# Kernel tuning notes

Hardware: AMD Instinct MI355X
Metric: run time of the kernel (lower is better)

## Reference

```python
import jax, jax.numpy as jnp
import numpy as np

VOCAB = 32000
HID = 1024
HEADS = 16
HEAD_DIM = HID // HEADS
LAYERS = 8
INTER = 4 * HID
ROPE_BASE = 100000.0
EPS = 1e-5


def setup_inputs() -> dict:
    key = jax.random.key(0)
    ks = jax.random.split(key, 12)
    s = 0.02
    inp = {
        'input_ids': jax.random.randint(ks[0], (2, 2048), 0, VOCAB),
        'embed_W': jax.random.normal(ks[1], (VOCAB, HID), jnp.float32) * s,
        'Wq': jax.random.normal(ks[2], (LAYERS, HID, HID), jnp.float32) * s,
        'Wk': jax.random.normal(ks[3], (LAYERS, HID, HID), jnp.float32) * s,
        'Wv': jax.random.normal(ks[4], (LAYERS, HID, HID), jnp.float32) * s,
        'Wo': jax.random.normal(ks[5], (LAYERS, HID, HID), jnp.float32) * s,
        'Wg': jax.random.normal(ks[6], (LAYERS, HID, INTER), jnp.float32) * s,
        'Wu': jax.random.normal(ks[7], (LAYERS, HID, INTER), jnp.float32) * s,
        'Wd': jax.random.normal(ks[8], (LAYERS, INTER, HID), jnp.float32) * s,
        'norm1_w': jnp.ones((LAYERS, HID), jnp.float32),
        'norm2_w': jnp.ones((LAYERS, HID), jnp.float32),
        'final_norm_w': jnp.ones((HID,), jnp.float32),
        'head_W': jax.random.normal(ks[9], (HID, VOCAB), jnp.float32) * s,
    }
    return inp


def rms_norm(x, w):
    return x * jax.lax.rsqrt(jnp.mean(x * x, axis=-1, keepdims=True) + EPS) * w


def rope_tables(seq_len):
    freq = 1.0 / (ROPE_BASE ** (jnp.arange(0, HEAD_DIM, 2, dtype=jnp.float32) / HEAD_DIM))
    ang = jnp.arange(seq_len, dtype=jnp.float32)[:, None] * freq  # [S, d/2]
    cos = jnp.concatenate([jnp.cos(ang), jnp.cos(ang)], axis=-1)  # [S, d]
    sin = jnp.concatenate([jnp.sin(ang), jnp.sin(ang)], axis=-1)
    return cos, sin


def rotate_half(x):
    h = x.shape[-1] // 2
    return jnp.concatenate([-x[..., h:], x[..., :h]], axis=-1)


def apply_rope(q, k, cos, sin):
    # q,k: [B,S,H,D]; cos,sin: [S,D] -> broadcast over heads via [:,None,:]
    c = cos[:, None, :]
    s = sin[:, None, :]
    return q * c + rotate_half(q) * s, k * c + rotate_half(k) * s


def attention(x, wq, wk, wv, wo, cos, sin, causal_mask):
    B, S, _ = x.shape
    q = (x @ wq).reshape(B, S, HEADS, HEAD_DIM)
    k = (x @ wk).reshape(B, S, HEADS, HEAD_DIM)
    v = (x @ wv).reshape(B, S, HEADS, HEAD_DIM)
    q, k = apply_rope(q, k, cos, sin)
    scores = jnp.einsum('bqhd,bkhd->bhqk', q, k) / np.sqrt(HEAD_DIM)
    scores = jnp.clip(scores, -1000.0, 1000.0)
    scores = jnp.where(causal_mask, jnp.finfo(scores.dtype).min, scores)
    w = jax.nn.softmax(scores.astype(jnp.float32), axis=-1).astype(q.dtype)
    w = jnp.clip(w, 0.0, 1.0)
    ctx = jnp.einsum('bhqk,bkhd->bqhd', w, v).reshape(B, S, HID)
    return ctx @ wo


def reference(input_ids, embed_W, Wq, Wk, Wv, Wo, Wg, Wu, Wd, norm1_w, norm2_w, final_norm_w, head_W):
    B, S = input_ids.shape
    h = embed_W[input_ids]  # [B,S,HID]
    cos, sin = rope_tables(S)
    causal_mask = jnp.triu(jnp.ones((S, S), bool), k=1)[None, None]
    for l in range(LAYERS):
        h = h + attention(rms_norm(h, norm1_w[l]), Wq[l], Wk[l], Wv[l], Wo[l], cos, sin, causal_mask)
        hn = rms_norm(h, norm2_w[l])
        h = h + (jax.nn.silu(hn @ Wg[l]) * (hn @ Wu[l])) @ Wd[l]
    h = rms_norm(h, final_norm_w)
    logits = h @ head_W
    return logits, h
```

## Files before the change

kernel.cpp:

```cpp
#include <hip/hip_runtime.h>

#define T_TOK 4096
#define SEQ   2048
#define HID   1024
#define NH    16
#define HD    64
#define INTER 4096
#define NLAYER 8
#define VOCAB 32000

typedef short short8 __attribute__((ext_vector_type(8)));
typedef float f32x4  __attribute__((ext_vector_type(4)));

__device__ __forceinline__ unsigned short f2bf(float f){
  unsigned int u = __builtin_bit_cast(unsigned int, f);
  u += 0x7fffu + ((u >> 16) & 1u);
  return (unsigned short)(u >> 16);
}
__device__ __forceinline__ float bf2f(unsigned short b){
  unsigned int u = ((unsigned int)b) << 16;
  return __builtin_bit_cast(float, u);
}

#define GLOAD_LDS16(gsrc, ldst) \
  __builtin_amdgcn_global_load_lds((const __attribute__((address_space(1))) void*)(gsrc), \
                                   (__attribute__((address_space(3))) void*)(ldst), 16, 0, 0)

__global__ __launch_bounds__(256) void embed_kernel(const int* __restrict__ ids,
                                                    const float* __restrict__ W,
                                                    float* __restrict__ h){
  int i = blockIdx.x * 256 + threadIdx.x;
  int t = i >> 8, c = i & 255;
  ((float4*)h)[i] = ((const float4*)(W + (size_t)ids[t] * HID))[c];
}

__global__ __launch_bounds__(256) void rope_tab_kernel(float* __restrict__ cosT,
                                                       float* __restrict__ sinT){
  int i = blockIdx.x * 256 + threadIdx.x;
  int s = i >> 5, f = i & 31;
  float inv = expf(-((2.0f * (float)f) / 64.0f) * logf(100000.0f));
  float ang = (float)s * inv;
  cosT[i] = cosf(ang);
  sinT[i] = sinf(ang);
}

__global__ __launch_bounds__(256) void rmsnorm_kernel(const float* __restrict__ h,
                                                      const float* __restrict__ w,
                                                      unsigned short* __restrict__ out,
                                                      float* hcopy){
  int t = blockIdx.x, tid = threadIdx.x;
  float4 v = ((const float4*)(h + (size_t)t * HID))[tid];
  float ss = v.x*v.x + v.y*v.y + v.z*v.z + v.w*v.w;
  #pragma unroll
  for (int m = 1; m < 64; m <<= 1) ss += __shfl_xor(ss, m);
  __shared__ float red[4];
  if ((tid & 63) == 0) red[tid >> 6] = ss;
  __syncthreads();
  float r = rsqrtf((red[0] + red[1] + red[2] + red[3]) * (1.0f / HID) + 1e-5f);
  float4 wv = ((const float4*)w)[tid];
  float nx = v.x * r * wv.x;
  float ny = v.y * r * wv.y;
  float nz = v.z * r * wv.z;
  float nw = v.w * r * wv.w;
  ushort4 o;
  o.x = f2bf(nx); o.y = f2bf(ny); o.z = f2bf(nz); o.w = f2bf(nw);
  ((ushort4*)(out + (size_t)t * HID))[tid] = o;
  if (hcopy){
    float4 hv; hv.x = nx; hv.y = ny; hv.z = nz; hv.w = nw;
    ((float4*)(hcopy + (size_t)t * HID))[tid] = hv;
  }
}

__global__ __launch_bounds__(256) void rope_kernel(unsigned short* __restrict__ q,
                                                   unsigned short* __restrict__ k,
                                                   const float* __restrict__ cosT,
                                                   const float* __restrict__ sinT){
  int i = blockIdx.x * 256 + threadIdx.x;
  int t = i >> 9, rem = i & 511;
  int hh = rem >> 5, f = rem & 31;
  int s = t & (SEQ - 1);
  float c = cosT[s * 32 + f], sn = sinT[s * 32 + f];
  size_t base = (size_t)t * HID + hh * HD + f;
  float q0 = bf2f(q[base]), q1 = bf2f(q[base + 32]);
  q[base]      = f2bf((q0 * c - q1 * sn) * 0.125f);
  q[base + 32] = f2bf((q1 * c + q0 * sn) * 0.125f);
  float k0 = bf2f(k[base]), k1 = bf2f(k[base + 32]);
  k[base]      = f2bf(k0 * c - k1 * sn);
  k[base + 32] = f2bf(k1 * c + k0 * sn);
}

__global__ __launch_bounds__(256) void convert_w_kernel(const float* __restrict__ W,
                                                        unsigned short* __restrict__ Wt,
                                                        int K, int N){
  __shared__ unsigned short t_lds[64][72];
  W  += (size_t)blockIdx.z * K * N;
  Wt += (size_t)blockIdx.z * K * N;
  const int n0 = blockIdx.x * 64, k0 = blockIdx.y * 64;
  const int tid = threadIdx.x;
  const int tr = tid >> 4, tc = tid & 15;
  #pragma unroll
  for (int i = 0; i < 4; ++i){
    int kk = tr + i * 16;
    float4 v = *(const float4*)(W + (size_t)(k0 + kk) * N + n0 + tc * 4);
    t_lds[tc*4+0][kk] = f2bf(v.x);
    t_lds[tc*4+1][kk] = f2bf(v.y);
    t_lds[tc*4+2][kk] = f2bf(v.z);
    t_lds[tc*4+3][kk] = f2bf(v.w);
  }
  __syncthreads();
  const int n = tid >> 2, cp = tid & 3;
  #pragma unroll
  for (int j = 0; j < 2; ++j){
    int c = cp * 2 + j;
    uint4 d = *(const uint4*)(&t_lds[n][c * 8]);
    *(uint4*)(Wt + (size_t)(n0 + n) * K + k0 + c * 8) = d;
  }
}

__device__ __forceinline__ void gemm_core(const unsigned short* __restrict__ A,
                                          const unsigned short* __restrict__ Bt,
                                          int Kstride, int Klen, int m0, int n0,
                                          unsigned short* As, unsigned short* Bs,
                                          f32x4 (&acc)[4][4]){
  const int tid = threadIdx.x;
  const int lane = tid & 63, w = tid >> 6;
  const int l15 = lane & 15, g = lane >> 4;
  const int wr = w >> 1, wc = w & 1;
  const int srow = lane >> 2;
  const int schunk = (((lane & 3) ^ ((srow >> 1) & 3)) << 3);
  const int sx = (l15 >> 1) & 3;

  #pragma unroll
  for (int m = 0; m < 4; ++m)
    #pragma unroll
    for (int n = 0; n < 4; ++n)
      #pragma unroll
      for (int i = 0; i < 4; ++i) acc[m][n][i] = 0.0f;

  for (int kk = 0; kk < Klen; kk += 32){
    __syncthreads();
    GLOAD_LDS16(A  + (size_t)(m0 +      w*16 + srow) * Kstride + kk + schunk, As + (w*16) * 32);
    GLOAD_LDS16(A  + (size_t)(m0 + 64 + w*16 + srow) * Kstride + kk + schunk, As + (64 + w*16) * 32);
    GLOAD_LDS16(Bt + (size_t)(n0 +      w*16 + srow) * Kstride + kk + schunk, Bs + (w*16) * 32);
    GLOAD_LDS16(Bt + (size_t)(n0 + 64 + w*16 + srow) * Kstride + kk + schunk, Bs + (64 + w*16) * 32);
    __syncthreads();
    short8 a[4], b[4];
    #pragma unroll
    for (int m = 0; m < 4; ++m)
      a[m] = *(const short8*)(As + (wr*64 + m*16 + l15) * 32 + ((g ^ sx) << 3));
    #pragma unroll
    for (int n = 0; n < 4; ++n)
      b[n] = *(const short8*)(Bs + (wc*64 + n*16 + l15) * 32 + ((g ^ sx) << 3));
    #pragma unroll
    for (int m = 0; m < 4; ++m)
      #pragma unroll
      for (int n = 0; n < 4; ++n)
        acc[m][n] = __builtin_amdgcn_mfma_f32_16x16x32_bf16(a[m], b[n], acc[m][n], 0, 0, 0);
  }
}

template<int MODE>
__device__ __forceinline__ void gemm_epi(const f32x4 (&acc)[4][4], void* Cout,
                                         const float* __restrict__ resid,
                                         int N, int m0, int n0, int ldt){
  const int tid = threadIdx.x;
  const int lane = tid & 63, w = tid >> 6;
  const int l15 = lane & 15, g = lane >> 4;
  const int wr = w >> 1, wc = w & 1;
  #pragma unroll
  for (int m = 0; m < 4; ++m){
    #pragma unroll
    for (int n = 0; n < 4; ++n){
      int row0 = m0 + wr * 64 + m * 16 + g * 4;
      int col  = n0 + wc * 64 + n * 16 + l15;
      #pragma unroll
      for (int i = 0; i < 4; ++i){
        float v = acc[m][n][i];
        if (MODE == 0){
          ((unsigned short*)Cout)[(size_t)(row0 + i) * N + col] = f2bf(v);
        } else if (MODE == 1){
          size_t idx = (size_t)(row0 + i) * N + col;
          ((float*)Cout)[idx] = resid[idx] + v;
        } else if (MODE == 2){
          ((unsigned short*)Cout)[(size_t)col * ldt + (row0 + i)] = f2bf(v);
        } else if (MODE == 3){
          __builtin_nontemporal_store(v, &((float*)Cout)[(size_t)(row0 + i) * N + col]);
        } else {
          atomicAdd(&((float*)Cout)[(size_t)(row0 + i) * N + col], v);
        }
      }
    }
  }
}

template<int MODE>
__global__ __launch_bounds__(256) void gemm_bf16(const unsigned short* __restrict__ A,
                                                 const unsigned short* __restrict__ Bt,
                                                 void* Cout, const float* resid,
                                                 int K, int N, int ldt){
  __shared__ unsigned short As[128 * 32];
  __shared__ unsigned short Bs[128 * 32];
  f32x4 acc[4][4];
  gemm_core(A, Bt, K, K, blockIdx.x * 128, blockIdx.y * 128, As, Bs, acc);
  gemm_epi<MODE>(acc, Cout, resid, N, blockIdx.x * 128, blockIdx.y * 128, ldt);
}

__global__ __launch_bounds__(256) void gemm_splitk(const unsigned short* __restrict__ A,
                                                   const unsigned short* __restrict__ Bt,
                                                   float* Cacc, int Kfull, int N){
  __shared__ unsigned short As[128 * 32];
  __shared__ unsigned short Bs[128 * 32];
  const int kh = blockIdx.z, khalf = Kfull >> 1;
  f32x4 acc[4][4];
  gemm_core(A + kh * khalf, Bt + kh * khalf, Kfull, khalf,
            blockIdx.x * 128, blockIdx.y * 128, As, Bs, acc);
  gemm_epi<4>(acc, Cacc, nullptr, N, blockIdx.x * 128, blockIdx.y * 128, 0);
}

__global__ __launch_bounds__(256) void gemm_qkv(const unsigned short* __restrict__ A,
                                                const unsigned short* __restrict__ BtQ,
                                                const unsigned short* __restrict__ BtK,
                                                const unsigned short* __restrict__ BtV,
                                                unsigned short* qb, unsigned short* kb,
                                                unsigned short* vt){
  __shared__ unsigned short As[128 * 32];
  __shared__ unsigned short Bs[128 * 32];
  const int nb = blockIdx.y, sel = nb >> 3, n0 = (nb & 7) * 128;
  const unsigned short* Bt = (sel == 0) ? BtQ : (sel == 1) ? BtK : BtV;
  f32x4 acc[4][4];
  gemm_core(A, Bt, HID, HID, blockIdx.x * 128, n0, As, Bs, acc);
  if (sel == 0)      gemm_epi<0>(acc, qb, nullptr, HID, blockIdx.x * 128, n0, 0);
  else if (sel == 1) gemm_epi<0>(acc, kb, nullptr, HID, blockIdx.x * 128, n0, 0);
  else               gemm_epi<2>(acc, vt, nullptr, HID, blockIdx.x * 128, n0, T_TOK);
}

__global__ __launch_bounds__(256) void gemm_gu(const unsigned short* __restrict__ A,
                                               const unsigned short* __restrict__ BtG,
                                               const unsigned short* __restrict__ BtU,
                                               unsigned short* gb, unsigned short* ub){
  __shared__ unsigned short As[128 * 32];
  __shared__ unsigned short Bs[128 * 32];
  const int nb = blockIdx.y, sel = nb >> 5, n0 = (nb & 31) * 128;
  f32x4 acc[4][4];
  gemm_core(A, sel ? BtU : BtG, HID, HID, blockIdx.x * 128, n0, As, Bs, acc);
  gemm_epi<0>(acc, sel ? ub : gb, nullptr, INTER, blockIdx.x * 128, n0, 0);
}

__global__ __launch_bounds__(256, 2) void gemm_f32b(const unsigned short* __restrict__ A,
                                                    const float* __restrict__ Bw,
                                                    float* __restrict__ Cout,
                                                    int M, int N, int K){
  __shared__ unsigned short As[128 * 32];
  __shared__ unsigned short Bs[128 * 32];
  const int tid = threadIdx.x;
  const int lane = tid & 63, wid = tid >> 6;
  const int l15 = lane & 15, g = lane >> 4;
  const int wr = wid >> 1, wc = wid & 1;
  const int m0 = blockIdx.x * 128, n0 = blockIdx.y * 128;
  const int bcol = tid & 127, bhalf = tid >> 7;
  f32x4 acc[4][4];
  #pragma unroll
  for (int m = 0; m < 4; ++m)
    #pragma unroll
    for (int n = 0; n < 4; ++n)
      #pragma unroll
      for (int i = 0; i < 4; ++i) acc[m][n][i] = 0.0f;
  for (int kk = 0; kk < K; kk += 32){
    __syncthreads();
    #pragma unroll
    for (int cc = 0; cc < 2; ++cc){
      int c = tid + cc * 256;
      int row = c >> 2, kc = (c & 3) << 3;
      uint4 d = *(const uint4*)(A + (size_t)(m0 + row) * K + kk + kc);
      *(uint4*)(&As[row * 32 + kc]) = d;
    }
    {
      const float* bp = Bw + (size_t)(kk + bhalf * 16) * N + n0 + bcol;
      float f[16];
      #pragma unroll
      for (int j = 0; j < 16; ++j) f[j] = bp[(size_t)j * N];
      unsigned int pk[8];
      #pragma unroll
      for (int j = 0; j < 8; ++j)
        pk[j] = (unsigned int)f2bf(f[2*j]) | ((unsigned int)f2bf(f[2*j+1]) << 16);
      int sw = (bcol >> 1) & 3;
      int c0 = ((bhalf << 1)     ) ^ sw;
      int c1 = ((bhalf << 1) | 1 ) ^ sw;
      uint4 w0; w0.x = pk[0]; w0.y = pk[1]; w0.z = pk[2]; w0.w = pk[3];
      uint4 w1; w1.x = pk[4]; w1.y = pk[5]; w1.z = pk[6]; w1.w = pk[7];
      *(uint4*)(&Bs[bcol * 32 + c0 * 8]) = w0;
      *(uint4*)(&Bs[bcol * 32 + c1 * 8]) = w1;
    }
    __syncthreads();
    short8 a[4], b[4];
    #pragma unroll
    for (int m = 0; m < 4; ++m)
      a[m] = *(const short8*)(&As[(wr*64 + m*16 + l15) * 32 + g*8]);
    #pragma unroll
    for (int n = 0; n < 4; ++n){
      int col = wc*64 + n*16 + l15;
      b[n] = *(const short8*)(&Bs[col * 32 + (g ^ ((col >> 1) & 3)) * 8]);
    }
    #pragma unroll
    for (int m = 0; m < 4; ++m)
      #pragma unroll
      for (int n = 0; n < 4; ++n)
        acc[m][n] = __builtin_amdgcn_mfma_f32_16x16x32_bf16(a[m], b[n], acc[m][n], 0, 0, 0);
  }
  #pragma unroll
  for (int m = 0; m < 4; ++m)
    #pragma unroll
    for (int n = 0; n < 4; ++n){
      int row0 = m0 + wr*64 + m*16 + g*4;
      int col  = n0 + wc*64 + n*16 + l15;
      #pragma unroll
      for (int i = 0; i < 4; ++i)
        Cout[(size_t)(row0 + i) * N + col] = acc[m][n][i];
    }
}

__global__ __launch_bounds__(256) void attn_kernel(const unsigned short* __restrict__ q,
                                                   const unsigned short* __restrict__ k,
                                                   const unsigned short* __restrict__ vt,
                                                   unsigned short* __restrict__ ctx){
  const int tid = threadIdx.x;
  const int lane = tid & 63, w = tid >> 6;
  const int l15 = lane & 15, g = lane >> 4;
  const int bx = (int)gridDim.x - 1 - (int)blockIdx.x;
  const int q0 = bx * 128 + w * 32;
  const int hh = blockIdx.y;
  const int tb = blockIdx.z * SEQ;

  __shared__ unsigned short Ks[64][72];
  __shared__ unsigned short Vs[64][72];
  __shared__ unsigned short Ps[4][16][72];

  short8 qa[2][2];
  #pragma unroll
  for (int qs = 0; qs < 2; ++qs)
    #pragma unroll
    for (int kd = 0; kd < 2; ++kd)
      qa[qs][kd] = *(const short8*)(q + (size_t)(tb + q0 + qs*16 + l15) * HID + hh*HD + kd*32 + g*8);

  float m_run[2][4], l_run[2][4];
  f32x4 o_acc[2][4];
  #pragma unroll
  for (int qs = 0; qs < 2; ++qs)
    #pragma unroll
    for (int i = 0; i < 4; ++i){ m_run[qs][i] = -1e30f; l_run[qs][i] = 0.0f; }
  #pragma unroll
  for (int qs = 0; qs < 2; ++qs)
    #pragma unroll
    for (int dt = 0; dt < 4; ++dt)
      #pragma unroll
      for (int i = 0; i < 4; ++i) o_acc[qs][dt][i] = 0.0f;

  const int ntile = 2 * bx + 2;
  const int srow = tid >> 2, sc = (tid & 3) * 16;
  const unsigned short* kbase = k  + (size_t)(tb + srow) * HID + hh*HD + sc;
  const unsigned short* vbase = vt + (size_t)(hh*HD + srow) * T_TOK + tb + sc;

  for (int kt = 0; kt < ntile; ++kt){
    const int kv0 = kt * 64;
    __syncthreads();
    {
      const unsigned short* kp = kbase + (size_t)kv0 * HID;
      const unsigned short* vp = vbase + kv0;
      *(uint4*)(&Ks[srow][sc])     = *(const uint4*)(kp);
      *(uint4*)(&Ks[srow][sc + 8]) = *(const uint4*)(kp + 8);
      *(uint4*)(&Vs[srow][sc])     = *(const uint4*)(vp);
      *(uint4*)(&Vs[srow][sc + 8]) = *(const uint4*)(vp + 8);
    }
    __syncthreads();
    const int nct = min(4, ((q0 + 31 - kv0) >> 4) + 1);
    if (nct <= 0) continue;
    const int nks = nct >> 1;

    #pragma unroll
    for (int qs = 0; qs < 2; ++qs){
      float pv[4][4];
      #pragma unroll
      for (int ct = 0; ct < 4; ++ct){
        if (ct < nct){
          f32x4 scv;
          #pragma unroll
          for (int i = 0; i < 4; ++i) scv[i] = 0.0f;
          scv = __builtin_amdgcn_mfma_f32_16x16x32_bf16(qa[qs][0],
                  *(const short8*)(&Ks[ct*16 + l15][g*8]), scv, 0, 0, 0);
          scv = __builtin_amdgcn_mfma_f32_16x16x32_bf16(qa[qs][1],
                  *(const short8*)(&Ks[ct*16 + l15][32 + g*8]), scv, 0, 0, 0);
          #pragma unroll
          for (int i = 0; i < 4; ++i){
            float s = fminf(fmaxf(scv[i], -1000.0f), 1000.0f);
            int row = q0 + qs*16 + g*4 + i;
            int col = kv0 + ct*16 + l15;
            pv[ct][i] = (col > row) ? -1e30f : s;
          }
        } else {
          #pragma unroll
          for (int i = 0; i < 4; ++i) pv[ct][i] = -1e30f;
        }
      }
      #pragma unroll
      for (int i = 0; i < 4; ++i){
        float mx = fmaxf(fmaxf(pv[0][i], pv[1][i]), fmaxf(pv[2][i], pv[3][i]));
        #pragma unroll
        for (int msk = 1; msk < 16; msk <<= 1) mx = fmaxf(mx, __shfl_xor(mx, msk));
        if (!__all(mx <= m_run[qs][i] + 8.0f)){
          float mnew = fmaxf(m_run[qs][i], mx);
          float scale = __expf(m_run[qs][i] - mnew);
          m_run[qs][i] = mnew;
          l_run[qs][i] *= scale;
          #pragma unroll
          for (int dt = 0; dt < 4; ++dt) o_acc[qs][dt][i] *= scale;
        }
        float psum = 0.0f;
        #pragma unroll
        for (int ct = 0; ct < 4; ++ct){
          if (ct < nct){
            float p = __expf(pv[ct][i] - m_run[qs][i]);
            pv[ct][i] = p; psum += p;
          } else pv[ct][i] = 0.0f;
        }
        #pragma unroll
        for (int msk = 1; msk < 16; msk <<= 1) psum += __shfl_xor(psum, msk);
        l_run[qs][i] += psum;
      }
      #pragma unroll
      for (int ct = 0; ct < 4; ++ct)
        if (ct < nct)
          #pragma unroll
          for (int i = 0; i < 4; ++i)
            Ps[w][g*4 + i][ct*16 + l15] = f2bf(pv[ct][i]);
      #pragma unroll
      for (int ks = 0; ks < 2; ++ks){
        if (ks < nks){
          short8 ap = *(const short8*)(&Ps[w][l15][ks*32 + g*8]);
          #pragma unroll
          for (int dt = 0; dt < 4; ++dt){
            short8 vb = *(const short8*)(&Vs[dt*16 + l15][ks*32 + g*8]);
            o_acc[qs][dt] = __builtin_amdgcn_mfma_f32_16x16x32_bf16(ap, vb, o_acc[qs][dt], 0, 0, 0);
          }
        }
      }
    }
  }
  #pragma unroll
  for (int qs = 0; qs < 2; ++qs)
    #pragma unroll
    for (int dt = 0; dt < 4; ++dt)
      #pragma unroll
      for (int i = 0; i < 4; ++i){
        float o = o_acc[qs][dt][i] / l_run[qs][i];
        ctx[(size_t)(tb + q0 + qs*16 + g*4 + i) * HID + hh*HD + dt*16 + l15] = f2bf(o);
      }
}

__global__ __launch_bounds__(256) void silu_mul_kernel(unsigned short* __restrict__ gbuf,
                                                       const unsigned short* __restrict__ ubuf){
  int i = blockIdx.x * 256 + threadIdx.x;
  ushort4 gv = ((const ushort4*)gbuf)[i];
  ushort4 uv = ((const ushort4*)ubuf)[i];
  ushort4 o;
  float x;
  x = bf2f(gv.x); o.x = f2bf((x / (1.0f + __expf(-x))) * bf2f(uv.x));
  x = bf2f(gv.y); o.y = f2bf((x / (1.0f + __expf(-x))) * bf2f(uv.y));
  x = bf2f(gv.z); o.z = f2bf((x / (1.0f + __expf(-x))) * bf2f(uv.z));
  x = bf2f(gv.w); o.w = f2bf((x / (1.0f + __expf(-x))) * bf2f(uv.w));
  ((ushort4*)gbuf)[i] = o;
}

extern "C" void kernel_launch(void* const* d_in, const int* in_sizes, int n_in,
                              void* d_out, int out_size, void* d_ws, size_t ws_size,
                              hipStream_t stream){
  const int*   ids    = (const int*)d_in[0];
  const float* embedW = (const float*)d_in[1];
  const float* Wq = (const float*)d_in[2];
  const float* Wk = (const float*)d_in[3];
  const float* Wv = (const float*)d_in[4];
  const float* Wo = (const float*)d_in[5];
  const float* Wg = (const float*)d_in[6];
  const float* Wu = (const float*)d_in[7];
  const float* Wd = (const float*)d_in[8];
  const float* n1 = (const float*)d_in[9];
  const float* n2 = (const float*)d_in[10];
  const float* nf = (const float*)d_in[11];
  const float* Wh = (const float*)d_in[12];
  float* out = (float*)d_out;

  char* scb = (char*)d_out;
  unsigned short* qb  = (unsigned short*)(scb + 0);
  unsigned short* kb  = (unsigned short*)(scb + 8388608);
  unsigned short* vtb = (unsigned short*)(scb + 16777216);
  unsigned short* ctx = (unsigned short*)(scb + 25165824);
  unsigned short* gb  = (unsigned short*)(scb + 33554432);
  unsigned short* ub  = (unsigned short*)(scb + 67108864);
  float* cosT = (float*)(scb + 100663296);
  float* sinT = (float*)(scb + 100925440);
  float* h_fallback   = (float*)(scb + 104857600);
  unsigned short* WtQ = (unsigned short*)(scb + 134217728);
  unsigned short* WtK = (unsigned short*)(scb + 150994944);
  unsigned short* WtV = (unsigned short*)(scb + 167772160);
  unsigned short* WtO = (unsigned short*)(scb + 184549376);
  unsigned short* WtG = (unsigned short*)(scb + 201326592);
  unsigned short* WtU = (unsigned short*)(scb + 268435456);
  unsigned short* WtD = (unsigned short*)(scb + 335544320);

  unsigned short* xn = (unsigned short*)d_ws;
  float* h = (ws_size >= 25165824u) ? (float*)((char*)d_ws + 8388608) : h_fallback;
  unsigned short* WhT = (ws_size >= 90701824u)
                      ? (unsigned short*)((char*)d_ws + 25165824) : nullptr;

  convert_w_kernel<<<dim3(16, 16, 8), 256, 0, stream>>>(Wq, WtQ, HID, HID);
  convert_w_kernel<<<dim3(16, 16, 8), 256, 0, stream>>>(Wk, WtK, HID, HID);
  convert_w_kernel<<<dim3(16, 16, 8), 256, 0, stream>>>(Wv, WtV, HID, HID);
  convert_w_kernel<<<dim3(16, 16, 8), 256, 0, stream>>>(Wo, WtO, HID, HID);
  convert_w_kernel<<<dim3(64, 16, 8), 256, 0, stream>>>(Wg, WtG, HID, INTER);
  convert_w_kernel<<<dim3(64, 16, 8), 256, 0, stream>>>(Wu, WtU, HID, INTER);
  convert_w_kernel<<<dim3(16, 64, 8), 256, 0, stream>>>(Wd, WtD, INTER, HID);
  if (WhT)
    convert_w_kernel<<<dim3(500, 16, 1), 256, 0, stream>>>(Wh, WhT, HID, VOCAB);

  embed_kernel<<<4096, 256, 0, stream>>>(ids, embedW, h);
  rope_tab_kernel<<<256, 256, 0, stream>>>(cosT, sinT);

  for (int l = 0; l < NLAYER; ++l){
    rmsnorm_kernel<<<4096, 256, 0, stream>>>(h, n1 + l*HID, xn, nullptr);
    gemm_qkv<<<dim3(32, 24), 256, 0, stream>>>(xn, WtQ + (size_t)l*HID*HID,
                                               WtK + (size_t)l*HID*HID,
                                               WtV + (size_t)l*HID*HID, qb, kb, vtb);
    rope_kernel<<<8192, 256, 0, stream>>>(qb, kb, cosT, sinT);
    attn_kernel<<<dim3(16, 16, 2), 256, 0, stream>>>(qb, kb, vtb, ctx);
    gemm_splitk<<<dim3(32, 8, 2), 256, 0, stream>>>(ctx, WtO + (size_t)l*HID*HID,
                                                    h, HID, HID);
    rmsnorm_kernel<<<4096, 256, 0, stream>>>(h, n2 + l*HID, xn, nullptr);
    gemm_gu<<<dim3(32, 64), 256, 0, stream>>>(xn, WtG + (size_t)l*HID*INTER,
                                              WtU + (size_t)l*HID*INTER, gb, ub);
    silu_mul_kernel<<<16384, 256, 0, stream>>>(gb, ub);
    gemm_splitk<<<dim3(32, 8, 2), 256, 0, stream>>>(gb, WtD + (size_t)l*HID*INTER,
                                                    h, INTER, HID);
  }

  rmsnorm_kernel<<<4096, 256, 0, stream>>>(h, nf, xn, out + 131072000);
  if (WhT)
    gemm_bf16<3><<<dim3(32, 250), 256, 0, stream>>>(xn, WhT, out, nullptr, HID, VOCAB, 0);
  else
    gemm_f32b<<<dim3(32, 250), 256, 0, stream>>>(xn, Wh, out, T_TOK, VOCAB, HID);
}
```

Before: 4.089 ms.

## Use K=64 GEMM tiles with pre-swizzled weights, drop split-K atomics

Adds a GEMM core that stages 64-wide K slices per iteration, which halves the number of barrier pairs. The weights are stored pre-swizzled at conversion time so the B tile can be loaded linearly into LDS without bank conflicts, while A is swizzled at load. The O-projection and down-projection switch from split-K with atomicAdd to a single pass with a fused residual add. The LM head grid is reordered so blocks sweep the vocab dimension first. In exchange, LDS use doubles and the two residual GEMMs launch only 256 blocks each, which lowers parallelism.

```diff
diff --git a/kernel.cpp b/kernel.cpp
--- a/kernel.cpp
+++ b/kernel.cpp
@@ -89,9 +89,9 @@
   k[base + 32] = f2bf(k1 * c + k0 * sn);
 }
 
-__global__ __launch_bounds__(256) void convert_w_kernel(const float* __restrict__ W,
-                                                        unsigned short* __restrict__ Wt,
-                                                        int K, int N){
+__global__ __launch_bounds__(256) void convert_w_swz(const float* __restrict__ W,
+                                                     unsigned short* __restrict__ Wt,
+                                                     int K, int N){
   __shared__ unsigned short t_lds[64][72];
   W  += (size_t)blockIdx.z * K * N;
   Wt += (size_t)blockIdx.z * K * N;
@@ -113,15 +113,94 @@
   for (int j = 0; j < 2; ++j){
     int c = cp * 2 + j;
     uint4 d = *(const uint4*)(&t_lds[n][c * 8]);
+    *(uint4*)(Wt + (size_t)(n0 + n) * K + k0 + ((c ^ (n & 7)) << 3)) = d;
+  }
+}
+
+__global__ __launch_bounds__(256) void convert_w_lin(const float* __restrict__ W,
+                                                     unsigned short* __restrict__ Wt,
+                                                     int K, int N){
+  __shared__ unsigned short t_lds[64][72];
+  const int n0 = blockIdx.x * 64, k0 = blockIdx.y * 64;
+  const int tid = threadIdx.x;
+  const int tr = tid >> 4, tc = tid & 15;
+  #pragma unroll
+  for (int i = 0; i < 4; ++i){
+    int kk = tr + i * 16;
+    float4 v = *(const float4*)(W + (size_t)(k0 + kk) * N + n0 + tc * 4);
+    t_lds[tc*4+0][kk] = f2bf(v.x);
+    t_lds[tc*4+1][kk] = f2bf(v.y);
+    t_lds[tc*4+2][kk] = f2bf(v.z);
+    t_lds[tc*4+3][kk] = f2bf(v.w);
+  }
+  __syncthreads();
+  const int n = tid >> 2, cp = tid & 3;
+  #pragma unroll
+  for (int j = 0; j < 2; ++j){
+    int c = cp * 2 + j;
+    uint4 d = *(const uint4*)(&t_lds[n][c * 8]);
     *(uint4*)(Wt + (size_t)(n0 + n) * K + k0 + c * 8) = d;
   }
 }
 
-__device__ __forceinline__ void gemm_core(const unsigned short* __restrict__ A,
-                                          const unsigned short* __restrict__ Bt,
-                                          int Kstride, int Klen, int m0, int n0,
-                                          unsigned short* As, unsigned short* Bs,
-                                          f32x4 (&acc)[4][4]){
+__device__ __forceinline__ void gemm_core64(const unsigned short* __restrict__ A,
+                                            const unsigned short* __restrict__ Bt,
+                                            int K, int m0, int n0,
+                                            unsigned short* As, unsigned short* Bs,
+                                            f32x4 (&acc)[4][4]){
+  const int tid = threadIdx.x;
+  const int lane = tid & 63, w = tid >> 6;
+  const int l15 = lane & 15, g = lane >> 4;
+  const int lr = lane >> 3;
+  const int lc = lane & 7;
+  const int wr = w >> 1, wc = w & 1;
+  const int axor = ((lc ^ lr) << 3);
+
+  #pragma unroll
+  for (int m = 0; m < 4; ++m)
+    #pragma unroll
+    for (int n = 0; n < 4; ++n)
+      #pragma unroll
+      for (int i = 0; i < 4; ++i) acc[m][n][i] = 0.0f;
+
+  for (int kk = 0; kk < K; kk += 64){
+    __syncthreads();
+    #pragma unroll
+    for (int i = 0; i < 4; ++i){
+      int rb = (i * 4 + w) * 8;
+      GLOAD_LDS16(A  + (size_t)(m0 + rb + lr) * K + kk + axor,      As + rb * 64);
+      GLOAD_LDS16(Bt + (size_t)(n0 + rb + lr) * K + kk + (lc << 3), Bs + rb * 64);
+    }
+    __syncthreads();
+    short8 a[4][2], b[4][2];
+    const int x = l15 & 7;
+    #pragma unroll
+    for (int m = 0; m < 4; ++m){
+      int row = wr * 64 + m * 16 + l15;
+      a[m][0] = *(const short8*)(As + row * 64 + ((g       ^ x) << 3));
+      a[m][1] = *(const short8*)(As + row * 64 + (((4 + g) ^ x) << 3));
+    }
+    #pragma unroll
+    for (int n = 0; n < 4; ++n){
+      int row = wc * 64 + n * 16 + l15;
+      b[n][0] = *(const short8*)(Bs + row * 64 + ((g       ^ x) << 3));
+      b[n][1] = *(const short8*)(Bs + row * 64 + (((4 + g) ^ x) << 3));
+    }
+    #pragma unroll
+    for (int m = 0; m < 4; ++m)
+      #pragma unroll
+      for (int n = 0; n < 4; ++n){
+        acc[m][n] = __builtin_amdgcn_mfma_f32_16x16x32_bf16(a[m][0], b[n][0], acc[m][n], 0, 0, 0);
+        acc[m][n] = __builtin_amdgcn_mfma_f32_16x16x32_bf16(a[m][1], b[n][1], acc[m][n], 0, 0, 0);
+      }
+  }
+}
+
+__device__ __forceinline__ void gemm_core32(const unsigned short* __restrict__ A,
+                                            const unsigned short* __restrict__ Bt,
+                                            int K, int m0, int n0,
+                                            unsigned short* As, unsigned short* Bs,
+                                            f32x4 (&acc)[4][4]){
   const int tid = threadIdx.x;
   const int lane = tid & 63, w = tid >> 6;
   const int l15 = lane & 15, g = lane >> 4;
@@ -137,12 +216,12 @@
       #pragma unroll
       for (int i = 0; i < 4; ++i) acc[m][n][i] = 0.0f;
 
-  for (int kk = 0; kk < Klen; kk += 32){
-    __syncthreads();
-    GLOAD_LDS16(A  + (size_t)(m0 +      w*16 + srow) * Kstride + kk + schunk, As + (w*16) * 32);
-    GLOAD_LDS16(A  + (size_t)(m0 + 64 + w*16 + srow) * Kstride + kk + schunk, As + (64 + w*16) * 32);
-    GLOAD_LDS16(Bt + (size_t)(n0 +      w*16 + srow) * Kstride + kk + schunk, Bs + (w*16) * 32);
-    GLOAD_LDS16(Bt + (size_t)(n0 + 64 + w*16 + srow) * Kstride + kk + schunk, Bs + (64 + w*16) * 32);
+  for (int kk = 0; kk < K; kk += 32){
+    __syncthreads();
+    GLOAD_LDS16(A  + (size_t)(m0 +      w*16 + srow) * K + kk + schunk, As + (w*16) * 32);
+    GLOAD_LDS16(A  + (size_t)(m0 + 64 + w*16 + srow) * K + kk + schunk, As + (64 + w*16) * 32);
+    GLOAD_LDS16(Bt + (size_t)(n0 +      w*16 + srow) * K + kk + schunk, Bs + (w*16) * 32);
+    GLOAD_LDS16(Bt + (size_t)(n0 + 64 + w*16 + srow) * K + kk + schunk, Bs + (64 + w*16) * 32);
     __syncthreads();
     short8 a[4], b[4];
     #pragma unroll
@@ -183,10 +262,8 @@
           ((float*)Cout)[idx] = resid[idx] + v;
         } else if (MODE == 2){
           ((unsigned short*)Cout)[(size_t)col * ldt + (row0 + i)] = f2bf(v);
-        } else if (MODE == 3){
+        } else {
           __builtin_nontemporal_store(v, &((float*)Cout)[(size_t)(row0 + i) * N + col]);
-        } else {
-          atomicAdd(&((float*)Cout)[(size_t)(row0 + i) * N + col], v);
         }
       }
     }
@@ -194,27 +271,15 @@
 }
 
 template<int MODE>
-__global__ __launch_bounds__(256) void gemm_bf16(const unsigned short* __restrict__ A,
-                                                 const unsigned short* __restrict__ Bt,
-                                                 void* Cout, const float* resid,
-                                                 int K, int N, int ldt){
-  __shared__ unsigned short As[128 * 32];
-  __shared__ unsigned short Bs[128 * 32];
+__global__ __launch_bounds__(256) void gemm64_k(const unsigned short* __restrict__ A,
+                                                const unsigned short* __restrict__ Bt,
+                                                void* Cout, const float* resid,
+                                                int K, int N, int ldt){
+  __shared__ unsigned short As[128 * 64];
+  __shared__ unsigned short Bs[128 * 64];
   f32x4 acc[4][4];
-  gemm_core(A, Bt, K, K, blockIdx.x * 128, blockIdx.y * 128, As, Bs, acc);
+  gemm_core64(A, Bt, K, blockIdx.x * 128, blockIdx.y * 128, As, Bs, acc);
   gemm_epi<MODE>(acc, Cout, resid, N, blockIdx.x * 128, blockIdx.y * 128, ldt);
-}
-
-__global__ __launch_bounds__(256) void gemm_splitk(const unsigned short* __restrict__ A,
-                                                   const unsigned short* __restrict__ Bt,
-                                                   float* Cacc, int Kfull, int N){
-  __shared__ unsigned short As[128 * 32];
-  __shared__ unsigned short Bs[128 * 32];
-  const int kh = blockIdx.z, khalf = Kfull >> 1;
-  f32x4 acc[4][4];
-  gemm_core(A + kh * khalf, Bt + kh * khalf, Kfull, khalf,
-            blockIdx.x * 128, blockIdx.y * 128, As, Bs, acc);
-  gemm_epi<4>(acc, Cacc, nullptr, N, blockIdx.x * 128, blockIdx.y * 128, 0);
 }
 
 __global__ __launch_bounds__(256) void gemm_qkv(const unsigned short* __restrict__ A,
@@ -223,12 +288,12 @@
                                                 const unsigned short* __restrict__ BtV,
                                                 unsigned short* qb, unsigned short* kb,
                                                 unsigned short* vt){
-  __shared__ unsigned short As[128 * 32];
-  __shared__ unsigned short Bs[128 * 32];
+  __shared__ unsigned short As[128 * 64];
+  __shared__ unsigned short Bs[128 * 64];
   const int nb = blockIdx.y, sel = nb >> 3, n0 = (nb & 7) * 128;
   const unsigned short* Bt = (sel == 0) ? BtQ : (sel == 1) ? BtK : BtV;
   f32x4 acc[4][4];
-  gemm_core(A, Bt, HID, HID, blockIdx.x * 128, n0, As, Bs, acc);
+  gemm_core64(A, Bt, HID, blockIdx.x * 128, n0, As, Bs, acc);
   if (sel == 0)      gemm_epi<0>(acc, qb, nullptr, HID, blockIdx.x * 128, n0, 0);
   else if (sel == 1) gemm_epi<0>(acc, kb, nullptr, HID, blockIdx.x * 128, n0, 0);
   else               gemm_epi<2>(acc, vt, nullptr, HID, blockIdx.x * 128, n0, T_TOK);
@@ -238,12 +303,23 @@
                                                const unsigned short* __restrict__ BtG,
                                                const unsigned short* __restrict__ BtU,
                                                unsigned short* gb, unsigned short* ub){
+  __shared__ unsigned short As[128 * 64];
+  __shared__ unsigned short Bs[128 * 64];
+  const int nb = blockIdx.y, sel = nb >> 5, n0 = (nb & 31) * 128;
+  f32x4 acc[4][4];
+  gemm_core64(A, sel ? BtU : BtG, HID, blockIdx.x * 128, n0, As, Bs, acc);
+  gemm_epi<0>(acc, sel ? ub : gb, nullptr, INTER, blockIdx.x * 128, n0, 0);
+}
+
+__global__ __launch_bounds__(256) void gemm_head(const unsigned short* __restrict__ A,
+                                                 const unsigned short* __restrict__ Bt,
+                                                 float* __restrict__ out){
   __shared__ unsigned short As[128 * 32];
   __shared__ unsigned short Bs[128 * 32];
-  const int nb = blockIdx.y, sel = nb >> 5, n0 = (nb & 31) * 128;
+  const int m0 = blockIdx.y * 128, n0 = blockIdx.x * 128;
   f32x4 acc[4][4];
-  gemm_core(A, sel ? BtU : BtG, HID, HID, blockIdx.x * 128, n0, As, Bs, acc);
-  gemm_epi<0>(acc, sel ? ub : gb, nullptr, INTER, blockIdx.x * 128, n0, 0);
+  gemm_core32(A, Bt, HID, m0, n0, As, Bs, acc);
+  gemm_epi<3>(acc, out, nullptr, VOCAB, m0, n0, 0);
 }
 
 __global__ __launch_bounds__(256, 2) void gemm_f32b(const unsigned short* __restrict__ A,
@@ -511,15 +587,15 @@
   unsigned short* WhT = (ws_size >= 90701824u)
                       ? (unsigned short*)((char*)d_ws + 25165824) : nullptr;
 
-  convert_w_kernel<<<dim3(16, 16, 8), 256, 0, stream>>>(Wq, WtQ, HID, HID);
-  convert_w_kernel<<<dim3(16, 16, 8), 256, 0, stream>>>(Wk, WtK, HID, HID);
-  convert_w_kernel<<<dim3(16, 16, 8), 256, 0, stream>>>(Wv, WtV, HID, HID);
-  convert_w_kernel<<<dim3(16, 16, 8), 256, 0, stream>>>(Wo, WtO, HID, HID);
-  convert_w_kernel<<<dim3(64, 16, 8), 256, 0, stream>>>(Wg, WtG, HID, INTER);
-  convert_w_kernel<<<dim3(64, 16, 8), 256, 0, stream>>>(Wu, WtU, HID, INTER);
-  convert_w_kernel<<<dim3(16, 64, 8), 256, 0, stream>>>(Wd, WtD, INTER, HID);
+  convert_w_swz<<<dim3(16, 16, 8), 256, 0, stream>>>(Wq, WtQ, HID, HID);
+  convert_w_swz<<<dim3(16, 16, 8), 256, 0, stream>>>(Wk, WtK, HID, HID);
+  convert_w_swz<<<dim3(16, 16, 8), 256, 0, stream>>>(Wv, WtV, HID, HID);
+  convert_w_swz<<<dim3(16, 16, 8), 256, 0, stream>>>(Wo, WtO, HID, HID);
+  convert_w_swz<<<dim3(64, 16, 8), 256, 0, stream>>>(Wg, WtG, HID, INTER);
+  convert_w_swz<<<dim3(64, 16, 8), 256, 0, stream>>>(Wu, WtU, HID, INTER);
+  convert_w_swz<<<dim3(16, 64, 8), 256, 0, stream>>>(Wd, WtD, INTER, HID);
   if (WhT)
-    convert_w_kernel<<<dim3(500, 16, 1), 256, 0, stream>>>(Wh, WhT, HID, VOCAB);
+    convert_w_lin<<<dim3(500, 16, 1), 256, 0, stream>>>(Wh, WhT, HID, VOCAB);
 
   embed_kernel<<<4096, 256, 0, stream>>>(ids, embedW, h);
   rope_tab_kernel<<<256, 256, 0, stream>>>(cosT, sinT);
@@ -531,19 +607,19 @@
                                                WtV + (size_t)l*HID*HID, qb, kb, vtb);
     rope_kernel<<<8192, 256, 0, stream>>>(qb, kb, cosT, sinT);
     attn_kernel<<<dim3(16, 16, 2), 256, 0, stream>>>(qb, kb, vtb, ctx);
-    gemm_splitk<<<dim3(32, 8, 2), 256, 0, stream>>>(ctx, WtO + (size_t)l*HID*HID,
-                                                    h, HID, HID);
+    gemm64_k<1><<<dim3(32, 8), 256, 0, stream>>>(ctx, WtO + (size_t)l*HID*HID,
+                                                 h, h, HID, HID, 0);
     rmsnorm_kernel<<<4096, 256, 0, stream>>>(h, n2 + l*HID, xn, nullptr);
     gemm_gu<<<dim3(32, 64), 256, 0, stream>>>(xn, WtG + (size_t)l*HID*INTER,
                                               WtU + (size_t)l*HID*INTER, gb, ub);
     silu_mul_kernel<<<16384, 256, 0, stream>>>(gb, ub);
-    gemm_splitk<<<dim3(32, 8, 2), 256, 0, stream>>>(gb, WtD + (size_t)l*HID*INTER,
-                                                    h, INTER, HID);
+    gemm64_k<1><<<dim3(32, 8), 256, 0, stream>>>(gb, WtD + (size_t)l*HID*INTER,
+                                                 h, h, INTER, HID, 0);
   }
 
   rmsnorm_kernel<<<4096, 256, 0, stream>>>(h, nf, xn, out + 131072000);
   if (WhT)
-    gemm_bf16<3><<<dim3(32, 250), 256, 0, stream>>>(xn, WhT, out, nullptr, HID, VOCAB, 0);
+    gemm_head<<<dim3(250, 32), 256, 0, stream>>>(xn, WhT, out);
   else
     gemm_f32b<<<dim3(32, 250), 256, 0, stream>>>(xn, Wh, out, T_TOK, VOCAB, HID);
 }
```

Measured after the change: 4.027 ms. Within noise of the previous version (-1.5%).
